# Kernel tuning notes

Hardware: AMD Instinct MI355X
Metric: run time of the kernel (lower is better)

Reference implementation:

```python
import jax, jax.numpy as jnp
import numpy as np

B, T, Z, S, H = 32, 128, 100, 6, 64
F1, F2 = 512, 128


def setup_inputs() -> dict:
    key = jax.random.key(0)
    ks = jax.random.split(key, 11)
    g = lambda k, shape, sc: (jax.random.normal(k, shape, dtype=jnp.float32) * sc)
    return {
        "x": jax.random.normal(ks[0], (B, T, Z, S), dtype=jnp.float32),
        "W_ih": g(ks[1], (3 * H, S), 0.125),   # GRU input weights [r|z|n]
        "W_hh": g(ks[2], (3 * H, H), 0.125),   # GRU hidden weights [r|z|n]
        "b_ih": g(ks[3], (3 * H,), 0.125),
        "b_hh": g(ks[4], (3 * H,), 0.125),
        "w1": g(ks[5], (F1, H), 0.1),
        "b1": g(ks[6], (F1,), 0.1),
        "w2": g(ks[7], (F2, F1), 0.04),
        "b2": g(ks[8], (F2,), 0.04),
        "w3": g(ks[9], (1, F2), 0.09),
        "b3": g(ks[10], (1,), 0.09),
    }


def reference(x, W_ih, W_hh, b_ih, b_hh, w1, b1, w2, b2, w3, b3):
    b, t, z, s = x.shape
    h_dim = W_hh.shape[1]
    # Fuse the per-zone python loop into the batch dim, zone-major so the
    # final reshape matches torch.stack(a).view(-1, t, nzones).
    xm = jnp.transpose(x, (2, 0, 1, 3)).reshape(z * b, t, s)  # (ZB, T, S)
    # Precompute input projections for all timesteps (one big GEMM).
    gi_all = jnp.einsum('nts,gs->ntg', xm, W_ih) + b_ih        # (ZB, T, 3H)

    def step(h, gi):
        gh = h @ W_hh.T + b_hh
        r = jax.nn.sigmoid(gi[:, :h_dim] + gh[:, :h_dim])
        zg = jax.nn.sigmoid(gi[:, h_dim:2 * h_dim] + gh[:, h_dim:2 * h_dim])
        n = jnp.tanh(gi[:, 2 * h_dim:] + r * gh[:, 2 * h_dim:])
        h_new = (1.0 - zg) * n + zg * h
        return h_new, h_new

    h0 = jnp.zeros((z * b, h_dim), x.dtype)
    _, sx = jax.lax.scan(step, h0, jnp.swapaxes(gi_all, 0, 1))  # (T, ZB, H)
    sx = jnp.swapaxes(sx, 0, 1)                                  # (ZB, T, H)

    a1 = jax.nn.relu(sx @ w1.T + b1)
    a2 = jax.nn.relu(a1 @ w2.T + b2)
    a3 = a2 @ w3.T + b3                                          # (ZB, T, 1)
    return a3.reshape(-1, t, z)                                  # (B, T, Z)
```

## Files before the change

kernel.cpp:

```cpp
#include <hip/hip_runtime.h>
#include <stdint.h>

#define Tdim 128
#define Zdim 100
#define Sdim 6
#define Hdim 64
#define ZB   3200
#define F1   512
#define F2   128
#define Mrows (ZB * Tdim)

typedef _Float16 f16x8 __attribute__((ext_vector_type(8)));
typedef _Float16 f16x4 __attribute__((ext_vector_type(4)));
typedef float f32x4 __attribute__((ext_vector_type(4)));
typedef uint32_t u32x4 __attribute__((ext_vector_type(4)));

__device__ __forceinline__ float sigmoidf_fast(float x) {
  return 1.f / (1.f + __expf(-x));
}
__device__ __forceinline__ float tanhf_fast(float x) {
  return 1.f - 2.f / (__expf(2.f * x) + 1.f);
}

__global__ __launch_bounds__(256) void prep_kernel(
    const float* __restrict__ W_ih, const float* __restrict__ W_hh,
    const float* __restrict__ w1, const float* __restrict__ w2,
    _Float16* __restrict__ Wf, _Float16* __restrict__ w1p,
    _Float16* __restrict__ w2p) {
  int i = blockIdx.x * 256 + threadIdx.x;
  if (i < 192 * 96) {
    int g = i / 96, k = i - g * 96;
    float v = (k < 64) ? W_hh[g * 64 + k] : ((k < 70) ? W_ih[g * 6 + (k - 64)] : 0.f);
    Wf[i] = (_Float16)v;
  }
  int j = i - 192 * 96;
  if (j >= 0 && j < 16 * 32 * 72) {
    int kt = j / 2304, r = j - kt * 2304;
    int f1 = r / 72, h = r - f1 * 72;
    w1p[j] = (_Float16)((h < 64) ? w1[(kt * 32 + f1) * 64 + h] : 0.f);
  }
  int l = j - 16 * 32 * 72;
  if (l >= 0 && l < 16 * 128 * 40) {
    int kt = l / 5120, r = l - kt * 5120;
    int f2 = r / 40, k = r - f2 * 40;
    w2p[l] = (_Float16)((k < 32) ? w2[f2 * 512 + kt * 32 + k] : 0.f);
  }
}

__global__ __launch_bounds__(256, 1) void gru_kernel(
    const float* __restrict__ x, const _Float16* __restrict__ Wf,
    const float* __restrict__ b_ih, const float* __restrict__ b_hh,
    _Float16* __restrict__ sx) {
  __shared__ _Float16 h16[2][16][72];
  const int tid = threadIdx.x;
  const int lane = tid & 63;
  const int w = tid >> 6;
  const int c = lane & 15;
  const int q = lane >> 4;

  const int gr0 = w * 16;
  const int gz0 = 64 + w * 16;
  const int gn0 = 128 + w * 16;

  f16x8 Ar[3], Az[3], Anh[2], Ani;
#pragma unroll
  for (int kf = 0; kf < 3; kf++) {
    Ar[kf] = *(const f16x8*)(Wf + (size_t)(gr0 + c) * 96 + kf * 32 + q * 8);
    Az[kf] = *(const f16x8*)(Wf + (size_t)(gz0 + c) * 96 + kf * 32 + q * 8);
  }
  Anh[0] = *(const f16x8*)(Wf + (size_t)(gn0 + c) * 96 + q * 8);
  Anh[1] = *(const f16x8*)(Wf + (size_t)(gn0 + c) * 96 + 32 + q * 8);
  Ani    = *(const f16x8*)(Wf + (size_t)(gn0 + c) * 96 + 64 + q * 8);

  f32x4 Cr, Cz, Cnh, Cni;
  {
    f32x4 bir = *(const f32x4*)(b_ih + gr0 + q * 4);
    f32x4 bhr = *(const f32x4*)(b_hh + gr0 + q * 4);
    f32x4 biz = *(const f32x4*)(b_ih + gz0 + q * 4);
    f32x4 bhz = *(const f32x4*)(b_hh + gz0 + q * 4);
#pragma unroll
    for (int r = 0; r < 4; r++) { Cr[r] = bir[r] + bhr[r]; Cz[r] = biz[r] + bhz[r]; }
    Cnh = *(const f32x4*)(b_hh + gn0 + q * 4);
    Cni = *(const f32x4*)(b_ih + gn0 + q * 4);
  }

  const int n = blockIdx.x * 16 + c;
  const int zz = n >> 5, bb = n & 31;
  const float* xp = x + (size_t)bb * (Tdim * Zdim * Sdim) + (size_t)zz * Sdim;
  _Float16* sxp = sx + (size_t)n * Tdim * Hdim;

  float xv[Sdim];
  if (q == 0) {
#pragma unroll
    for (int s = 0; s < Sdim; s++) xv[s] = xp[s];
  }

  f16x8 Bh0 = {0, 0, 0, 0, 0, 0, 0, 0};
  f16x8 Bh1 = {0, 0, 0, 0, 0, 0, 0, 0};
  f32x4 hprev = {0.f, 0.f, 0.f, 0.f};

  for (int t = 0; t < Tdim; t++) {
    f16x8 Bx = {0, 0, 0, 0, 0, 0, 0, 0};
    if (q == 0) {
      Bx[0] = (_Float16)xv[0]; Bx[1] = (_Float16)xv[1]; Bx[2] = (_Float16)xv[2];
      Bx[3] = (_Float16)xv[3]; Bx[4] = (_Float16)xv[4]; Bx[5] = (_Float16)xv[5];
    }
    f32x4 Dr = __builtin_amdgcn_mfma_f32_16x16x32_f16(Ar[0], Bh0, Cr, 0, 0, 0);
    f32x4 Dz = __builtin_amdgcn_mfma_f32_16x16x32_f16(Az[0], Bh0, Cz, 0, 0, 0);
    f32x4 Dnh = __builtin_amdgcn_mfma_f32_16x16x32_f16(Anh[0], Bh0, Cnh, 0, 0, 0);
    f32x4 Dni = __builtin_amdgcn_mfma_f32_16x16x32_f16(Ani, Bx, Cni, 0, 0, 0);
    Dr = __builtin_amdgcn_mfma_f32_16x16x32_f16(Ar[1], Bh1, Dr, 0, 0, 0);
    Dz = __builtin_amdgcn_mfma_f32_16x16x32_f16(Az[1], Bh1, Dz, 0, 0, 0);
    Dnh = __builtin_amdgcn_mfma_f32_16x16x32_f16(Anh[1], Bh1, Dnh, 0, 0, 0);
    Dr = __builtin_amdgcn_mfma_f32_16x16x32_f16(Ar[2], Bx, Dr, 0, 0, 0);
    Dz = __builtin_amdgcn_mfma_f32_16x16x32_f16(Az[2], Bx, Dz, 0, 0, 0);

    if (q == 0 && t + 1 < Tdim) {
      const float* p = xp + (size_t)(t + 1) * (Zdim * Sdim);
#pragma unroll
      for (int s = 0; s < Sdim; s++) xv[s] = p[s];
    }

    f16x4 pk;
#pragma unroll
    for (int r = 0; r < 4; r++) {
      float rr = sigmoidf_fast(Dr[r]);
      float zg = sigmoidf_fast(Dz[r]);
      float nn = tanhf_fast(Dni[r] + rr * Dnh[r]);
      float hnew = nn + zg * (hprev[r] - nn);
      hprev[r] = hnew;
      pk[r] = (_Float16)hnew;
    }
    *(f16x4*)&h16[t & 1][c][w * 16 + q * 4] = pk;
    *(f16x4*)(sxp + t * Hdim + w * 16 + q * 4) = pk;
    __syncthreads();
    Bh0 = *(const f16x8*)&h16[t & 1][c][q * 8];
    Bh1 = *(const f16x8*)&h16[t & 1][c][32 + q * 8];
  }
}

__global__ __launch_bounds__(256, 3) void mlp_kernel(
    const _Float16* __restrict__ sx, const _Float16* __restrict__ w1p,
    const _Float16* __restrict__ w2p, const float* __restrict__ b1,
    const float* __restrict__ b2, const float* __restrict__ w3,
    const float* __restrict__ b3, float* __restrict__ out) {
  __shared__ __align__(16) _Float16 w1s[2][32][72];
  __shared__ __align__(16) _Float16 w2s[2][128][40];
  __shared__ __align__(16) _Float16 rep[4][2][2][16][36];
  const int tid = threadIdx.x;
  const int lane = tid & 63;
  const int wave = tid >> 6;
  const int c = lane & 15;
  const int q = lane >> 4;
  const size_t m0 = ((size_t)blockIdx.x * 4 + wave) * 32;

  f16x8 Bs[2][2];
#pragma unroll
  for (int g = 0; g < 2; g++)
#pragma unroll
    for (int kk = 0; kk < 2; kk++)
      Bs[g][kk] = *(const f16x8*)(sx + (m0 + g * 16 + c) * Hdim + kk * 32 + q * 8);

  f32x4 acc2[2][8];
#pragma unroll
  for (int g = 0; g < 2; g++)
#pragma unroll
    for (int nt = 0; nt < 8; nt++) acc2[g][nt] = (f32x4){0.f, 0.f, 0.f, 0.f};

  u32x4 r1a, r1b, r2a, r2b, r2c;
  {
    const u32x4* g1 = (const u32x4*)(w1p);
    const u32x4* g2 = (const u32x4*)(w2p);
    r1a = g1[tid];
    if (tid < 32) r1b = g1[256 + tid];
    r2a = g2[tid];
    r2b = g2[256 + tid];
    if (tid < 128) r2c = g2[512 + tid];
    u32x4* s1 = (u32x4*)&w1s[0][0][0];
    u32x4* s2 = (u32x4*)&w2s[0][0][0];
    s1[tid] = r1a;
    if (tid < 32) s1[256 + tid] = r1b;
    s2[tid] = r2a;
    s2[256 + tid] = r2b;
    if (tid < 128) s2[512 + tid] = r2c;
  }
  __syncthreads();

#pragma unroll 2
  for (int kt = 0; kt < 16; kt++) {
    const int buf = kt & 1;
    if (kt + 1 < 16) {
      const u32x4* g1 = (const u32x4*)(w1p + (size_t)(kt + 1) * 2304);
      const u32x4* g2 = (const u32x4*)(w2p + (size_t)(kt + 1) * 5120);
      r1a = g1[tid];
      if (tid < 32) r1b = g1[256 + tid];
      r2a = g2[tid];
      r2b = g2[256 + tid];
      if (tid < 128) r2c = g2[512 + tid];
    }

#pragma unroll
    for (int ntl = 0; ntl < 2; ntl++) {
      const int f1b = kt * 32 + ntl * 16;
      f16x8 A0 = *(const f16x8*)&w1s[buf][ntl * 16 + c][q * 8];
      f16x8 A1 = *(const f16x8*)&w1s[buf][ntl * 16 + c][32 + q * 8];
      f32x4 bb = *(const f32x4*)(b1 + f1b + q * 4);
#pragma unroll
      for (int g = 0; g < 2; g++) {
        f32x4 cc = {0.f, 0.f, 0.f, 0.f};
        cc = __builtin_amdgcn_mfma_f32_16x16x32_f16(A0, Bs[g][0], cc, 0, 0, 0);
        cc = __builtin_amdgcn_mfma_f32_16x16x32_f16(A1, Bs[g][1], cc, 0, 0, 0);
        f16x4 pk;
#pragma unroll
        for (int r = 0; r < 4; r++) {
          float v = cc[r] + bb[r];
          pk[r] = (_Float16)(v > 0.f ? v : 0.f);
        }
        *(f16x4*)&rep[wave][buf][g][c][ntl * 16 + q * 4] = pk;
      }
    }
    f16x8 Ba[2];
#pragma unroll
    for (int g = 0; g < 2; g++) {
      f16x4 lo = *(const f16x4*)&rep[wave][buf][g][c][q * 8];
      f16x4 hi = *(const f16x4*)&rep[wave][buf][g][c][q * 8 + 4];
#pragma unroll
      for (int j = 0; j < 4; j++) { Ba[g][j] = lo[j]; Ba[g][4 + j] = hi[j]; }
    }
#pragma unroll
    for (int nt = 0; nt < 8; nt++) {
      f16x8 A2 = *(const f16x8*)&w2s[buf][nt * 16 + c][q * 8];
#pragma unroll
      for (int g = 0; g < 2; g++)
        acc2[g][nt] = __builtin_amdgcn_mfma_f32_16x16x32_f16(A2, Ba[g], acc2[g][nt], 0, 0, 0);
    }

    if (kt + 1 < 16) {
      u32x4* s1 = (u32x4*)&w1s[buf ^ 1][0][0];
      u32x4* s2 = (u32x4*)&w2s[buf ^ 1][0][0];
      s1[tid] = r1a;
      if (tid < 32) s1[256 + tid] = r1b;
      s2[tid] = r2a;
      s2[256 + tid] = r2b;
      if (tid < 128) s2[512 + tid] = r2c;
      __syncthreads();
    }
  }

  float part[2] = {0.f, 0.f};
#pragma unroll
  for (int nt = 0; nt < 8; nt++) {
    f32x4 bb = *(const f32x4*)(b2 + nt * 16 + q * 4);
    f32x4 ww = *(const f32x4*)(w3 + nt * 16 + q * 4);
#pragma unroll
    for (int g = 0; g < 2; g++) {
#pragma unroll
      for (int r = 0; r < 4; r++) {
        float v = acc2[g][nt][r] + bb[r];
        v = v > 0.f ? v : 0.f;
        part[g] = fmaf(v, ww[r], part[g]);
      }
    }
  }
#pragma unroll
  for (int g = 0; g < 2; g++) {
    part[g] += __shfl_xor(part[g], 16, 64);
    part[g] += __shfl_xor(part[g], 32, 64);
  }
  if (q < 2) {
    float pv = (q == 0) ? part[0] : part[1];
    out[m0 + q * 16 + c] = pv + b3[0];
  }
}

extern "C" void kernel_launch(void* const* d_in, const int* in_sizes, int n_in,
                              void* d_out, int out_size, void* d_ws, size_t ws_size,
                              hipStream_t stream) {
  const float* x    = (const float*)d_in[0];
  const float* W_ih = (const float*)d_in[1];
  const float* W_hh = (const float*)d_in[2];
  const float* b_ih = (const float*)d_in[3];
  const float* b_hh = (const float*)d_in[4];
  const float* w1   = (const float*)d_in[5];
  const float* b1   = (const float*)d_in[6];
  const float* w2   = (const float*)d_in[7];
  const float* b2   = (const float*)d_in[8];
  const float* w3   = (const float*)d_in[9];
  const float* b3   = (const float*)d_in[10];
  float* out = (float*)d_out;

  char* ws = (char*)d_ws;
  _Float16* sxf = (_Float16*)ws;
  _Float16* Wf  = (_Float16*)(ws + 52428800);
  _Float16* w1p = (_Float16*)(ws + 52428800 + 36864);
  _Float16* w2p = (_Float16*)(ws + 52428800 + 36864 + 73728);

  hipLaunchKernelGGL(prep_kernel, dim3(536), dim3(256), 0, stream,
                     W_ih, W_hh, w1, w2, Wf, w1p, w2p);
  hipLaunchKernelGGL(gru_kernel, dim3(ZB / 16), dim3(256), 0, stream,
                     x, Wf, b_ih, b_hh, sxf);
  hipLaunchKernelGGL(mlp_kernel, dim3(Mrows / 128), dim3(256), 0, stream,
                     sxf, w1p, w2p, b1, b2, w3, b3, out);
}
```

Baseline: 258.9 us.

## Stage GRU outputs in LDS history and coalesce writes; fold biases into MFMA accumulators

The GRU kernel now keeps a 64-step history of hidden states in shared memory instead of a two-slot buffer. Every 64 steps it flushes that history to global memory with contiguous 16-byte stores, replacing the scattered 8-byte per-step stores. MFMAs that depend only on x are issued first, so they can run before the new hidden state arrives. The MLP folds b1 and b2 into the MFMA accumulator init, uses a single-buffered, wider-stride rep array so B fragments load as one f16x8, and raises the occupancy hint to 4. The cost is a much larger LDS footprint in the GRU kernel (about 147 KB) and an extra barrier at each flush.

```diff
diff --git a/kernel.cpp b/kernel.cpp
--- a/kernel.cpp
+++ b/kernel.cpp
@@ -51,7 +51,7 @@
     const float* __restrict__ x, const _Float16* __restrict__ Wf,
     const float* __restrict__ b_ih, const float* __restrict__ b_hh,
     _Float16* __restrict__ sx) {
-  __shared__ _Float16 h16[2][16][72];
+  __shared__ _Float16 hist[64][16][72];
   const int tid = threadIdx.x;
   const int lane = tid & 63;
   const int w = tid >> 6;
@@ -87,7 +87,6 @@
   const int n = blockIdx.x * 16 + c;
   const int zz = n >> 5, bb = n & 31;
   const float* xp = x + (size_t)bb * (Tdim * Zdim * Sdim) + (size_t)zz * Sdim;
-  _Float16* sxp = sx + (size_t)n * Tdim * Hdim;
 
   float xv[Sdim];
   if (q == 0) {
@@ -105,15 +104,15 @@
       Bx[0] = (_Float16)xv[0]; Bx[1] = (_Float16)xv[1]; Bx[2] = (_Float16)xv[2];
       Bx[3] = (_Float16)xv[3]; Bx[4] = (_Float16)xv[4]; Bx[5] = (_Float16)xv[5];
     }
-    f32x4 Dr = __builtin_amdgcn_mfma_f32_16x16x32_f16(Ar[0], Bh0, Cr, 0, 0, 0);
-    f32x4 Dz = __builtin_amdgcn_mfma_f32_16x16x32_f16(Az[0], Bh0, Cz, 0, 0, 0);
+    f32x4 Dni = __builtin_amdgcn_mfma_f32_16x16x32_f16(Ani, Bx, Cni, 0, 0, 0);
+    f32x4 Dr  = __builtin_amdgcn_mfma_f32_16x16x32_f16(Ar[2], Bx, Cr, 0, 0, 0);
+    f32x4 Dz  = __builtin_amdgcn_mfma_f32_16x16x32_f16(Az[2], Bx, Cz, 0, 0, 0);
     f32x4 Dnh = __builtin_amdgcn_mfma_f32_16x16x32_f16(Anh[0], Bh0, Cnh, 0, 0, 0);
-    f32x4 Dni = __builtin_amdgcn_mfma_f32_16x16x32_f16(Ani, Bx, Cni, 0, 0, 0);
-    Dr = __builtin_amdgcn_mfma_f32_16x16x32_f16(Ar[1], Bh1, Dr, 0, 0, 0);
-    Dz = __builtin_amdgcn_mfma_f32_16x16x32_f16(Az[1], Bh1, Dz, 0, 0, 0);
+    Dr  = __builtin_amdgcn_mfma_f32_16x16x32_f16(Ar[0], Bh0, Dr, 0, 0, 0);
+    Dz  = __builtin_amdgcn_mfma_f32_16x16x32_f16(Az[0], Bh0, Dz, 0, 0, 0);
     Dnh = __builtin_amdgcn_mfma_f32_16x16x32_f16(Anh[1], Bh1, Dnh, 0, 0, 0);
-    Dr = __builtin_amdgcn_mfma_f32_16x16x32_f16(Ar[2], Bx, Dr, 0, 0, 0);
-    Dz = __builtin_amdgcn_mfma_f32_16x16x32_f16(Az[2], Bx, Dz, 0, 0, 0);
+    Dr  = __builtin_amdgcn_mfma_f32_16x16x32_f16(Ar[1], Bh1, Dr, 0, 0, 0);
+    Dz  = __builtin_amdgcn_mfma_f32_16x16x32_f16(Az[1], Bh1, Dz, 0, 0, 0);
 
     if (q == 0 && t + 1 < Tdim) {
       const float* p = xp + (size_t)(t + 1) * (Zdim * Sdim);
@@ -131,22 +130,39 @@
       hprev[r] = hnew;
       pk[r] = (_Float16)hnew;
     }
-    *(f16x4*)&h16[t & 1][c][w * 16 + q * 4] = pk;
-    *(f16x4*)(sxp + t * Hdim + w * 16 + q * 4) = pk;
+    *(f16x4*)&hist[t & 63][c][w * 16 + q * 4] = pk;
     __syncthreads();
-    Bh0 = *(const f16x8*)&h16[t & 1][c][q * 8];
-    Bh1 = *(const f16x8*)&h16[t & 1][c][32 + q * 8];
-  }
-}
-
-__global__ __launch_bounds__(256, 3) void mlp_kernel(
+    Bh0 = *(const f16x8*)&hist[t & 63][c][q * 8];
+    Bh1 = *(const f16x8*)&hist[t & 63][c][32 + q * 8];
+
+    if ((t & 63) == 63) {
+      const int t0 = t - 63;
+#pragma unroll
+      for (int rr = 0; rr < 4; rr++) {
+        const int row = w * 4 + rr;
+        const int nrow = blockIdx.x * 16 + row;
+        _Float16* dst = sx + (size_t)nrow * Tdim * Hdim + (size_t)t0 * Hdim;
+#pragma unroll
+        for (int it = 0; it < 8; it++) {
+          int idx = it * 64 + lane;
+          int tc = idx >> 3, hd8 = idx & 7;
+          f16x8 v = *(const f16x8*)&hist[tc][row][hd8 * 8];
+          *(f16x8*)(dst + tc * 64 + hd8 * 8) = v;
+        }
+      }
+      __syncthreads();
+    }
+  }
+}
+
+__global__ __launch_bounds__(256, 4) void mlp_kernel(
     const _Float16* __restrict__ sx, const _Float16* __restrict__ w1p,
     const _Float16* __restrict__ w2p, const float* __restrict__ b1,
     const float* __restrict__ b2, const float* __restrict__ w3,
     const float* __restrict__ b3, float* __restrict__ out) {
   __shared__ __align__(16) _Float16 w1s[2][32][72];
   __shared__ __align__(16) _Float16 w2s[2][128][40];
-  __shared__ __align__(16) _Float16 rep[4][2][2][16][36];
+  __shared__ __align__(16) _Float16 rep[4][2][16][40];
   const int tid = threadIdx.x;
   const int lane = tid & 63;
   const int wave = tid >> 6;
@@ -163,9 +179,11 @@
 
   f32x4 acc2[2][8];
 #pragma unroll
-  for (int g = 0; g < 2; g++)
-#pragma unroll
-    for (int nt = 0; nt < 8; nt++) acc2[g][nt] = (f32x4){0.f, 0.f, 0.f, 0.f};
+  for (int nt = 0; nt < 8; nt++) {
+    f32x4 bb = *(const f32x4*)(b2 + nt * 16 + q * 4);
+    acc2[0][nt] = bb;
+    acc2[1][nt] = bb;
+  }
 
   u32x4 r1a, r1b, r2a, r2b, r2c;
   {
@@ -207,26 +225,19 @@
       f32x4 bb = *(const f32x4*)(b1 + f1b + q * 4);
 #pragma unroll
       for (int g = 0; g < 2; g++) {
-        f32x4 cc = {0.f, 0.f, 0.f, 0.f};
-        cc = __builtin_amdgcn_mfma_f32_16x16x32_f16(A0, Bs[g][0], cc, 0, 0, 0);
+        f32x4 cc = __builtin_amdgcn_mfma_f32_16x16x32_f16(A0, Bs[g][0], bb, 0, 0, 0);
         cc = __builtin_amdgcn_mfma_f32_16x16x32_f16(A1, Bs[g][1], cc, 0, 0, 0);
         f16x4 pk;
 #pragma unroll
-        for (int r = 0; r < 4; r++) {
-          float v = cc[r] + bb[r];
-          pk[r] = (_Float16)(v > 0.f ? v : 0.f);
-        }
-        *(f16x4*)&rep[wave][buf][g][c][ntl * 16 + q * 4] = pk;
+        for (int r = 0; r < 4; r++)
+          pk[r] = (_Float16)(cc[r] > 0.f ? cc[r] : 0.f);
+        *(f16x4*)&rep[wave][g][c][ntl * 16 + q * 4] = pk;
       }
     }
     f16x8 Ba[2];
 #pragma unroll
-    for (int g = 0; g < 2; g++) {
-      f16x4 lo = *(const f16x4*)&rep[wave][buf][g][c][q * 8];
-      f16x4 hi = *(const f16x4*)&rep[wave][buf][g][c][q * 8 + 4];
-#pragma unroll
-      for (int j = 0; j < 4; j++) { Ba[g][j] = lo[j]; Ba[g][4 + j] = hi[j]; }
-    }
+    for (int g = 0; g < 2; g++)
+      Ba[g] = *(const f16x8*)&rep[wave][g][c][q * 8];
 #pragma unroll
     for (int nt = 0; nt < 8; nt++) {
       f16x8 A2 = *(const f16x8*)&w2s[buf][nt * 16 + c][q * 8];
@@ -250,13 +261,12 @@
   float part[2] = {0.f, 0.f};
 #pragma unroll
   for (int nt = 0; nt < 8; nt++) {
-    f32x4 bb = *(const f32x4*)(b2 + nt * 16 + q * 4);
     f32x4 ww = *(const f32x4*)(w3 + nt * 16 + q * 4);
 #pragma unroll
     for (int g = 0; g < 2; g++) {
 #pragma unroll
       for (int r = 0; r < 4; r++) {
-        float v = acc2[g][nt][r] + bb[r];
+        float v = acc2[g][nt][r];
         v = v > 0.f ? v : 0.f;
         part[g] = fmaf(v, ww[r], part[g]);
       }
```

Result: slower. 294.6 us (+13.8%).

## Stage GRU inputs in LDS and batch hidden-state writes via 32-step history buffer

Applied to the files above, without the earlier changes.

The GRU kernel now preloads the whole x sequence for its 16 rows into shared memory as fp16 before the recurrence, which removes the per-step dependent global loads. Hidden states are kept in a 32-step shared history ring and flushed to global memory every 32 steps as coalesced 16-byte stores, replacing the scattered 8-byte stores issued each step. The MFMA order is also changed so the input-projection products, which do not depend on h, are issued first. In exchange the kernel uses more shared memory and adds an extra barrier at every flush.

```diff
diff --git a/kernel.cpp b/kernel.cpp
--- a/kernel.cpp
+++ b/kernel.cpp
@@ -51,12 +51,26 @@
     const float* __restrict__ x, const _Float16* __restrict__ Wf,
     const float* __restrict__ b_ih, const float* __restrict__ b_hh,
     _Float16* __restrict__ sx) {
-  __shared__ _Float16 h16[2][16][72];
+  __shared__ __align__(16) _Float16 hist[32][16][72];
+  __shared__ __align__(16) _Float16 xs[Tdim][16][8];
   const int tid = threadIdx.x;
   const int lane = tid & 63;
   const int w = tid >> 6;
   const int c = lane & 15;
   const int q = lane >> 4;
+
+  for (int i = 0; i < 8; i++) {
+    int idx = i * 256 + tid;
+    int t = idx >> 4, row = idx & 15;
+    int nr = blockIdx.x * 16 + row;
+    const float* p = x + (size_t)(nr & 31) * (Tdim * Zdim * Sdim)
+                       + (size_t)t * (Zdim * Sdim) + (size_t)(nr >> 5) * Sdim;
+    f16x8 v;
+    v[0] = (_Float16)p[0]; v[1] = (_Float16)p[1]; v[2] = (_Float16)p[2];
+    v[3] = (_Float16)p[3]; v[4] = (_Float16)p[4]; v[5] = (_Float16)p[5];
+    v[6] = (_Float16)0.f;  v[7] = (_Float16)0.f;
+    *(f16x8*)&xs[t][row][0] = v;
+  }
 
   const int gr0 = w * 16;
   const int gz0 = 64 + w * 16;
@@ -84,42 +98,28 @@
     Cni = *(const f32x4*)(b_ih + gn0 + q * 4);
   }
 
-  const int n = blockIdx.x * 16 + c;
-  const int zz = n >> 5, bb = n & 31;
-  const float* xp = x + (size_t)bb * (Tdim * Zdim * Sdim) + (size_t)zz * Sdim;
-  _Float16* sxp = sx + (size_t)n * Tdim * Hdim;
-
-  float xv[Sdim];
-  if (q == 0) {
-#pragma unroll
-    for (int s = 0; s < Sdim; s++) xv[s] = xp[s];
-  }
+  __syncthreads();
 
   f16x8 Bh0 = {0, 0, 0, 0, 0, 0, 0, 0};
   f16x8 Bh1 = {0, 0, 0, 0, 0, 0, 0, 0};
   f32x4 hprev = {0.f, 0.f, 0.f, 0.f};
 
   for (int t = 0; t < Tdim; t++) {
-    f16x8 Bx = {0, 0, 0, 0, 0, 0, 0, 0};
-    if (q == 0) {
-      Bx[0] = (_Float16)xv[0]; Bx[1] = (_Float16)xv[1]; Bx[2] = (_Float16)xv[2];
-      Bx[3] = (_Float16)xv[3]; Bx[4] = (_Float16)xv[4]; Bx[5] = (_Float16)xv[5];
-    }
-    f32x4 Dr = __builtin_amdgcn_mfma_f32_16x16x32_f16(Ar[0], Bh0, Cr, 0, 0, 0);
-    f32x4 Dz = __builtin_amdgcn_mfma_f32_16x16x32_f16(Az[0], Bh0, Cz, 0, 0, 0);
+    const int tc = t & 31;
+    f16x8 xv8 = *(const f16x8*)&xs[t][c][0];
+    f16x8 Bx;
+#pragma unroll
+    for (int j = 0; j < 8; j++) Bx[j] = (q == 0) ? xv8[j] : (_Float16)0.f;
+
+    f32x4 Dni = __builtin_amdgcn_mfma_f32_16x16x32_f16(Ani, Bx, Cni, 0, 0, 0);
+    f32x4 Dr  = __builtin_amdgcn_mfma_f32_16x16x32_f16(Ar[2], Bx, Cr, 0, 0, 0);
+    f32x4 Dz  = __builtin_amdgcn_mfma_f32_16x16x32_f16(Az[2], Bx, Cz, 0, 0, 0);
     f32x4 Dnh = __builtin_amdgcn_mfma_f32_16x16x32_f16(Anh[0], Bh0, Cnh, 0, 0, 0);
-    f32x4 Dni = __builtin_amdgcn_mfma_f32_16x16x32_f16(Ani, Bx, Cni, 0, 0, 0);
-    Dr = __builtin_amdgcn_mfma_f32_16x16x32_f16(Ar[1], Bh1, Dr, 0, 0, 0);
-    Dz = __builtin_amdgcn_mfma_f32_16x16x32_f16(Az[1], Bh1, Dz, 0, 0, 0);
+    Dr  = __builtin_amdgcn_mfma_f32_16x16x32_f16(Ar[0], Bh0, Dr, 0, 0, 0);
+    Dz  = __builtin_amdgcn_mfma_f32_16x16x32_f16(Az[0], Bh0, Dz, 0, 0, 0);
     Dnh = __builtin_amdgcn_mfma_f32_16x16x32_f16(Anh[1], Bh1, Dnh, 0, 0, 0);
-    Dr = __builtin_amdgcn_mfma_f32_16x16x32_f16(Ar[2], Bx, Dr, 0, 0, 0);
-    Dz = __builtin_amdgcn_mfma_f32_16x16x32_f16(Az[2], Bx, Dz, 0, 0, 0);
-
-    if (q == 0 && t + 1 < Tdim) {
-      const float* p = xp + (size_t)(t + 1) * (Zdim * Sdim);
-#pragma unroll
-      for (int s = 0; s < Sdim; s++) xv[s] = p[s];
-    }
+    Dr  = __builtin_amdgcn_mfma_f32_16x16x32_f16(Ar[1], Bh1, Dr, 0, 0, 0);
+    Dz  = __builtin_amdgcn_mfma_f32_16x16x32_f16(Az[1], Bh1, Dz, 0, 0, 0);
 
     f16x4 pk;
 #pragma unroll
@@ -131,11 +131,28 @@
       hprev[r] = hnew;
       pk[r] = (_Float16)hnew;
     }
-    *(f16x4*)&h16[t & 1][c][w * 16 + q * 4] = pk;
-    *(f16x4*)(sxp + t * Hdim + w * 16 + q * 4) = pk;
+    *(f16x4*)&hist[tc][c][w * 16 + q * 4] = pk;
     __syncthreads();
-    Bh0 = *(const f16x8*)&h16[t & 1][c][q * 8];
-    Bh1 = *(const f16x8*)&h16[t & 1][c][32 + q * 8];
+    Bh0 = *(const f16x8*)&hist[tc][c][q * 8];
+    Bh1 = *(const f16x8*)&hist[tc][c][32 + q * 8];
+
+    if (tc == 31) {
+      const int t0 = t - 31;
+#pragma unroll
+      for (int rr2 = 0; rr2 < 4; rr2++) {
+        const int row = w * 4 + rr2;
+        const int nrow = blockIdx.x * 16 + row;
+        _Float16* dst = sx + (size_t)nrow * Tdim * Hdim + (size_t)t0 * Hdim;
+#pragma unroll
+        for (int it = 0; it < 4; it++) {
+          int idx = it * 64 + lane;
+          int tcc = idx >> 3, hd8 = idx & 7;
+          f16x8 vv = *(const f16x8*)&hist[tcc][row][hd8 * 8];
+          *(f16x8*)(dst + tcc * 64 + hd8 * 8) = vv;
+        }
+      }
+      __syncthreads();
+    }
   }
 }
 
```

After: 260.9 us. Within noise of the previous version (+0.8%).
